# Optimization experiments

Measured on AMD Instinct MI355X. Metric: run time of the kernel, lower is better.

## Reference

```python
import jax, jax.numpy as jnp
import numpy as np

P = 2.0  # exponent from init kwarg p


def _segment_mean(vals, idx, n):
    # scatter-mean with zero for empty segments (matches torch_scatter reduce='mean')
    s = jax.ops.segment_sum(vals, idx, num_segments=n)
    c = jax.ops.segment_sum(jnp.ones((vals.shape[0], 1), vals.dtype), idx, num_segments=n)
    return s / jnp.maximum(c, 1.0)


def setup_inputs() -> dict:
    key = jax.random.key(0)
    ks = jax.random.split(key, 6)
    N, E, nhid, heads = 100000, 3200000, 64, 4
    X = jax.random.normal(ks[0], (N, nhid), dtype=jnp.float32)
    edge_index = jax.random.randint(ks[1], (2, E), 0, N, dtype=jnp.int32)
    s1 = 1.0 / np.sqrt(nhid)
    W_self = jax.random.normal(ks[2], (nhid, nhid), dtype=jnp.float32) * s1
    W_neigh = jax.random.normal(ks[3], (nhid, nhid), dtype=jnp.float32) * s1
    b_conv = jnp.zeros((nhid,), dtype=jnp.float32)
    s2 = 1.0 / np.sqrt(2 * nhid)
    Qw = jax.random.normal(ks[4], (heads, 2 * nhid, nhid // heads), dtype=jnp.float32) * s2
    Qb = jnp.zeros((heads, nhid // heads), dtype=jnp.float32)
    return {"X": X, "edge_index": edge_index, "W_self": W_self,
            "W_neigh": W_neigh, "b_conv": b_conv, "Qw": Qw, "Qb": Qb}


def reference(X, edge_index, W_self, W_neigh, b_conv, Qw, Qb):
    N = X.shape[0]
    src, dst = edge_index[0], edge_index[1]
    # GraphSAGE conv: self-linear + linear over mean of neighbor features, then ReLU
    agg = _segment_mean(X[src], dst, N)                     # [N, nhid]
    X2 = jax.nn.relu(X @ W_self + agg @ W_neigh + b_conv)   # [N, nhid]
    # gather both edge endpoints and concat
    ef = jnp.concatenate([X2[src], X2[dst]], axis=1)        # [E, 2*nhid]
    # per-head small linear, abs^p, heads concatenated -> [E, nhid]
    h = jnp.einsum('ef,hfd->ehd', ef, Qw) + Qb              # [E, heads, nhid/heads]
    h = (jnp.abs(h) ** P).reshape(ef.shape[0], -1)
    # scatter-mean by source node, tanh
    gg = jnp.tanh(_segment_mean(h, src, N))                 # [N, nhid]
    return gg
```

## Files before the change

### kernel.cpp

```cpp
#include <hip/hip_runtime.h>
#include <math.h>

#define NHID 64
#define NPB 512
#define NPB_SHIFT 9
#define MAXB 256
#define CAP 20480
#define CHUNK 8192

__device__ __forceinline__ float bf_lo(unsigned u) { return __uint_as_float(u << 16); }
__device__ __forceinline__ float bf_hi(unsigned u) { return __uint_as_float(u & 0xffff0000u); }
__device__ __forceinline__ unsigned f2bf(float f) {
    unsigned u = __float_as_uint(f);
    return (u + 0x7fffu + ((u >> 16) & 1u)) >> 16;
}

__global__ __launch_bounds__(256) void k_bucketA(const int* __restrict__ src,
                                                 const int* __restrict__ dst,
                                                 unsigned int* __restrict__ buf0,
                                                 unsigned int* __restrict__ buf1,
                                                 int* __restrict__ btail0,
                                                 int* __restrict__ btail1,
                                                 int E, int nB) {
    int side  = blockIdx.x & 1;
    int chunk = blockIdx.x >> 1;
    const int* key = side ? src : dst;
    const int* pay = side ? dst : src;
    unsigned int* buf = side ? buf1 : buf0;
    int* btail = side ? btail1 : btail0;

    __shared__ int h[MAXB], b[MAXB];
    int tid = threadIdx.x;
    for (int i = tid; i < nB; i += 256) h[i] = 0;
    __syncthreads();
    int e0 = chunk * CHUNK;
    for (int i = tid; i < CHUNK / 4; i += 256) {
        int e = e0 + i * 4;
        if (e + 3 < E) {
            int4 k4 = ((const int4*)(key + e0))[i];
            atomicAdd(&h[k4.x >> NPB_SHIFT], 1);
            atomicAdd(&h[k4.y >> NPB_SHIFT], 1);
            atomicAdd(&h[k4.z >> NPB_SHIFT], 1);
            atomicAdd(&h[k4.w >> NPB_SHIFT], 1);
        } else {
            for (int j = 0; j < 4; ++j) {
                int e2 = e + j;
                if (e2 < E) atomicAdd(&h[key[e2] >> NPB_SHIFT], 1);
            }
        }
    }
    __syncthreads();
    for (int i = tid; i < nB; i += 256) {
        int c = h[i];
        b[i] = c ? atomicAdd(&btail[i], c) : 0;
        h[i] = 0;
    }
    __syncthreads();
    for (int i = tid; i < CHUNK / 4; i += 256) {
        int e = e0 + i * 4;
        if (e + 3 < E) {
            int4 k4 = ((const int4*)(key + e0))[i];
            int4 p4 = ((const int4*)(pay + e0))[i];
            int bb, r;
            bb = k4.x >> NPB_SHIFT; r = atomicAdd(&h[bb], 1) + b[bb];
            if (r < CAP) buf[(size_t)bb * CAP + r] = ((unsigned)p4.x << NPB_SHIFT) | (unsigned)(k4.x & (NPB - 1));
            bb = k4.y >> NPB_SHIFT; r = atomicAdd(&h[bb], 1) + b[bb];
            if (r < CAP) buf[(size_t)bb * CAP + r] = ((unsigned)p4.y << NPB_SHIFT) | (unsigned)(k4.y & (NPB - 1));
            bb = k4.z >> NPB_SHIFT; r = atomicAdd(&h[bb], 1) + b[bb];
            if (r < CAP) buf[(size_t)bb * CAP + r] = ((unsigned)p4.z << NPB_SHIFT) | (unsigned)(k4.z & (NPB - 1));
            bb = k4.w >> NPB_SHIFT; r = atomicAdd(&h[bb], 1) + b[bb];
            if (r < CAP) buf[(size_t)bb * CAP + r] = ((unsigned)p4.w << NPB_SHIFT) | (unsigned)(k4.w & (NPB - 1));
        } else {
            for (int j = 0; j < 4; ++j) {
                int e2 = e + j;
                if (e2 < E) {
                    int k = key[e2], p = pay[e2];
                    int bb = k >> NPB_SHIFT;
                    int r = atomicAdd(&h[bb], 1) + b[bb];
                    if (r < CAP) buf[(size_t)bb * CAP + r] = ((unsigned)p << NPB_SHIFT) | (unsigned)(k & (NPB - 1));
                }
            }
        }
    }
}

__global__ __launch_bounds__(256) void k_bscan(const int* __restrict__ btail0,
                                               const int* __restrict__ btail1,
                                               int* __restrict__ boff0, int* __restrict__ boff1,
                                               int* __restrict__ off0, int* __restrict__ off1,
                                               int nB, int N) {
    __shared__ int sd[256];
    int tid = threadIdx.x;
    int v = (tid < nB) ? min(btail0[tid], CAP) : 0;
    sd[tid] = v; __syncthreads();
    for (int o = 1; o < 256; o <<= 1) {
        int t = (tid >= o) ? sd[tid - o] : 0; __syncthreads();
        sd[tid] += t; __syncthreads();
    }
    if (tid < nB) boff0[tid] = sd[tid] - v;
    if (tid == 255) off0[N] = sd[255];
    __syncthreads();
    v = (tid < nB) ? min(btail1[tid], CAP) : 0;
    sd[tid] = v; __syncthreads();
    for (int o = 1; o < 256; o <<= 1) {
        int t = (tid >= o) ? sd[tid - o] : 0; __syncthreads();
        sd[tid] += t; __syncthreads();
    }
    if (tid < nB) boff1[tid] = sd[tid] - v;
    if (tid == 255) off1[N] = sd[255];
}

__global__ __launch_bounds__(512) void k_bucket_csr(const unsigned int* __restrict__ buf0,
                                                    const unsigned int* __restrict__ buf1,
                                                    const int* __restrict__ btail0,
                                                    const int* __restrict__ btail1,
                                                    const int* __restrict__ boff0,
                                                    const int* __restrict__ boff1,
                                                    int* __restrict__ off0, int* __restrict__ off1,
                                                    int* __restrict__ csr0, int* __restrict__ csr1,
                                                    int N) {
    int side = blockIdx.x & 1;
    int b = blockIdx.x >> 1;
    const unsigned int* buf = (side ? buf1 : buf0) + (size_t)b * CAP;
    int cnt_b = min((side ? btail1 : btail0)[b], CAP);
    int boff  = (side ? boff1 : boff0)[b];
    int* off  = side ? off1 : off0;
    int* csr  = side ? csr1 : csr0;
    __shared__ int cnt[NPB];
    __shared__ int scn[NPB];
    __shared__ int cur[NPB];
    int tid = threadIdx.x;
    cnt[tid] = 0;
    __syncthreads();
    for (int i = tid; i < cnt_b; i += 512)
        atomicAdd(&cnt[buf[i] & (NPB - 1)], 1);
    __syncthreads();
    int v = cnt[tid];
    scn[tid] = v; __syncthreads();
    for (int o = 1; o < 512; o <<= 1) {
        int t = (tid >= o) ? scn[tid - o] : 0; __syncthreads();
        scn[tid] += t; __syncthreads();
    }
    int base = boff + scn[tid] - v;
    cur[tid] = base;
    int node = (b << NPB_SHIFT) + tid;
    if (node < N) off[node] = base;
    __syncthreads();
    for (int i = tid; i < cnt_b; i += 512) {
        unsigned int u = buf[i];
        int pos = atomicAdd(&cur[u & (NPB - 1)], 1);
        csr[pos] = (int)(u >> NPB_SHIFT);
    }
}

__global__ __launch_bounds__(256) void k_xcast(const float* __restrict__ X,
                                               unsigned* __restrict__ Xb, int total8) {
    int i = blockIdx.x * 256 + threadIdx.x;
    if (i >= total8) return;
    const float4* Xv = (const float4*)X;
    float4 f0 = Xv[(size_t)i * 2];
    float4 f1 = Xv[(size_t)i * 2 + 1];
    uint4 p;
    p.x = f2bf(f0.x) | (f2bf(f0.y) << 16);
    p.y = f2bf(f0.z) | (f2bf(f0.w) << 16);
    p.z = f2bf(f1.x) | (f2bf(f1.y) << 16);
    p.w = f2bf(f1.z) | (f2bf(f1.w) << 16);
    ((uint4*)Xb)[i] = p;
}

#define AGG_ACC(u) \
    accA.x += bf_lo(u.x); accA.y += bf_hi(u.x); \
    accA.z += bf_lo(u.y); accA.w += bf_hi(u.y); \
    accB.x += bf_lo(u.z); accB.y += bf_hi(u.z); \
    accB.z += bf_lo(u.w); accB.w += bf_hi(u.w);
#define AGG_ACCM(u, f) \
    accA.x += f * bf_lo(u.x); accA.y += f * bf_hi(u.x); \
    accA.z += f * bf_lo(u.y); accA.w += f * bf_hi(u.y); \
    accB.x += f * bf_lo(u.z); accB.y += f * bf_hi(u.z); \
    accB.z += f * bf_lo(u.w); accB.w += f * bf_hi(u.w);

__global__ __launch_bounds__(256) void k_agg(const unsigned* __restrict__ Xb,
                                             const int* __restrict__ off_dst,
                                             const int* __restrict__ csr_dst,
                                             float* __restrict__ agg, int N) {
    int lane = threadIdx.x & 63;
    int node = blockIdx.x * 4 + (threadIdx.x >> 6);
    if (node >= N) return;
    int grp = lane >> 3, col8 = lane & 7;
    const uint4* Xb4 = (const uint4*)Xb;
    int s0 = off_dst[node], s1 = off_dst[node + 1];
    float4 accA = make_float4(0.f, 0.f, 0.f, 0.f);
    float4 accB = make_float4(0.f, 0.f, 0.f, 0.f);
    for (int base = s0; base < s1; base += 64) {
        int cnt = min(64, s1 - base);
        int idx = (base + lane < s1) ? csr_dst[base + lane] : 0;
        int j = 0;
        for (; j + 32 <= cnt; j += 32) {
            int m0 = __shfl(idx, j + grp);
            int m1 = __shfl(idx, j + 8 + grp);
            int m2 = __shfl(idx, j + 16 + grp);
            int m3 = __shfl(idx, j + 24 + grp);
            uint4 u0 = Xb4[(size_t)m0 * 8 + col8];
            uint4 u1 = Xb4[(size_t)m1 * 8 + col8];
            uint4 u2 = Xb4[(size_t)m2 * 8 + col8];
            uint4 u3 = Xb4[(size_t)m3 * 8 + col8];
            AGG_ACC(u0); AGG_ACC(u1); AGG_ACC(u2); AGG_ACC(u3);
        }
        if (j < cnt) {
            int q0 = j + grp, q1 = j + 8 + grp, q2 = j + 16 + grp, q3 = j + 24 + grp;
            int m0 = __shfl(idx, q0);
            int m1 = __shfl(idx, q1);
            int m2 = __shfl(idx, q2);
            int m3 = __shfl(idx, q3);
            float f0 = (q0 < cnt) ? 1.f : 0.f; if (q0 >= cnt) m0 = 0;
            float f1 = (q1 < cnt) ? 1.f : 0.f; if (q1 >= cnt) m1 = 0;
            float f2 = (q2 < cnt) ? 1.f : 0.f; if (q2 >= cnt) m2 = 0;
            float f3 = (q3 < cnt) ? 1.f : 0.f; if (q3 >= cnt) m3 = 0;
            uint4 u0 = Xb4[(size_t)m0 * 8 + col8];
            uint4 u1 = Xb4[(size_t)m1 * 8 + col8];
            uint4 u2 = Xb4[(size_t)m2 * 8 + col8];
            uint4 u3 = Xb4[(size_t)m3 * 8 + col8];
            AGG_ACCM(u0, f0); AGG_ACCM(u1, f1); AGG_ACCM(u2, f2); AGG_ACCM(u3, f3);
        }
    }
    #pragma unroll
    for (int d = 8; d < 64; d <<= 1) {
        accA.x += __shfl_xor(accA.x, d); accA.y += __shfl_xor(accA.y, d);
        accA.z += __shfl_xor(accA.z, d); accA.w += __shfl_xor(accA.w, d);
        accB.x += __shfl_xor(accB.x, d); accB.y += __shfl_xor(accB.y, d);
        accB.z += __shfl_xor(accB.z, d); accB.w += __shfl_xor(accB.w, d);
    }
    if (grp == 0) {
        int deg = s1 - s0;
        float inv = 1.f / (float)max(deg, 1);
        float4 r0 = make_float4(accA.x * inv, accA.y * inv, accA.z * inv, accA.w * inv);
        float4 r1 = make_float4(accB.x * inv, accB.y * inv, accB.z * inv, accB.w * inv);
        ((float4*)agg)[(size_t)node * 16 + col8 * 2]     = r0;
        ((float4*)agg)[(size_t)node * 16 + col8 * 2 + 1] = r1;
    }
}

__global__ __launch_bounds__(256) void k_phaseA(const float* __restrict__ X,
                                                const float* __restrict__ agg,
                                                const float* __restrict__ Ws,
                                                const float* __restrict__ Wn,
                                                const float* __restrict__ bconv,
                                                unsigned* __restrict__ X2b, int N) {
    __shared__ float sWs[4096];
    __shared__ float sWn[4096];
    __shared__ float sb[64];
    int tid = threadIdx.x;
    for (int i = tid; i < 4096; i += 256) {
        sWs[i] = Ws[i];
        sWn[i] = Wn[i];
    }
    if (tid < 64) sb[tid] = bconv[tid];
    __syncthreads();

    int n = blockIdx.x * 64 + (tid >> 2);
    if (n >= N) return;
    int wb = (tid & 3) << 2;
    const float4* ws4 = (const float4*)sWs;
    const float4* wn4 = (const float4*)sWn;
    const float4* bv  = (const float4*)sb;
    const float4* Xv  = (const float4*)(X + (size_t)n * NHID);
    const float4* Gv  = (const float4*)(agg + (size_t)n * NHID);
    float4 a0 = bv[wb], a1 = bv[wb + 1], a2 = bv[wb + 2], a3 = bv[wb + 3];
    #pragma unroll 2
    for (int q = 0; q < 16; ++q) {
        float4 xq = Xv[q];
        float4 gq = Gv[q];
        float xs[4] = {xq.x, xq.y, xq.z, xq.w};
        float gs[4] = {gq.x, gq.y, gq.z, gq.w};
        #pragma unroll
        for (int j = 0; j < 4; ++j) {
            int k16 = (4 * q + j) * 16 + wb;
            float4 w0 = ws4[k16], w1 = ws4[k16 + 1], w2 = ws4[k16 + 2], w3 = ws4[k16 + 3];
            float4 m0 = wn4[k16], m1 = wn4[k16 + 1], m2 = wn4[k16 + 2], m3 = wn4[k16 + 3];
            float xj = xs[j], gj = gs[j];
            a0.x += xj * w0.x + gj * m0.x; a0.y += xj * w0.y + gj * m0.y;
            a0.z += xj * w0.z + gj * m0.z; a0.w += xj * w0.w + gj * m0.w;
            a1.x += xj * w1.x + gj * m1.x; a1.y += xj * w1.y + gj * m1.y;
            a1.z += xj * w1.z + gj * m1.z; a1.w += xj * w1.w + gj * m1.w;
            a2.x += xj * w2.x + gj * m2.x; a2.y += xj * w2.y + gj * m2.y;
            a2.z += xj * w2.z + gj * m2.z; a2.w += xj * w2.w + gj * m2.w;
            a3.x += xj * w3.x + gj * m3.x; a3.y += xj * w3.y + gj * m3.y;
            a3.z += xj * w3.z + gj * m3.z; a3.w += xj * w3.w + gj * m3.w;
        }
    }
    a0.x = fmaxf(a0.x, 0.f); a0.y = fmaxf(a0.y, 0.f); a0.z = fmaxf(a0.z, 0.f); a0.w = fmaxf(a0.w, 0.f);
    a1.x = fmaxf(a1.x, 0.f); a1.y = fmaxf(a1.y, 0.f); a1.z = fmaxf(a1.z, 0.f); a1.w = fmaxf(a1.w, 0.f);
    a2.x = fmaxf(a2.x, 0.f); a2.y = fmaxf(a2.y, 0.f); a2.z = fmaxf(a2.z, 0.f); a2.w = fmaxf(a2.w, 0.f);
    a3.x = fmaxf(a3.x, 0.f); a3.y = fmaxf(a3.y, 0.f); a3.z = fmaxf(a3.z, 0.f); a3.w = fmaxf(a3.w, 0.f);
    uint4 p0, p1;
    p0.x = f2bf(a0.x) | (f2bf(a0.y) << 16);
    p0.y = f2bf(a0.z) | (f2bf(a0.w) << 16);
    p0.z = f2bf(a1.x) | (f2bf(a1.y) << 16);
    p0.w = f2bf(a1.z) | (f2bf(a1.w) << 16);
    p1.x = f2bf(a2.x) | (f2bf(a2.y) << 16);
    p1.y = f2bf(a2.z) | (f2bf(a2.w) << 16);
    p1.z = f2bf(a3.x) | (f2bf(a3.y) << 16);
    p1.w = f2bf(a3.z) | (f2bf(a3.w) << 16);
    uint4* outp = (uint4*)X2b + (size_t)n * 8 + (tid & 3) * 2;
    outp[0] = p0; outp[1] = p1;
}

__global__ __launch_bounds__(256) void k_repackB(const float* __restrict__ Qw,
                                                 float* __restrict__ W2) {
    int i = blockIdx.x * 256 + threadIdx.x;
    if (i >= 8192) return;
    int f = i >> 7, c = i & 127;
    float v;
    if (c < 64) v = Qw[(c >> 4) * 2048 + f * 16 + (c & 15)];
    else { int cc = c - 64; v = Qw[(cc >> 4) * 2048 + (64 + f) * 16 + (cc & 15)]; }
    W2[i] = v;
}

__global__ __launch_bounds__(256) void k_phaseB(const unsigned* __restrict__ X2b,
                                                const float* __restrict__ W2,
                                                const float* __restrict__ Qb,
                                                unsigned* __restrict__ aOut,
                                                unsigned* __restrict__ bOut, int N) {
    __shared__ float sW[10240];
    int tid = threadIdx.x;
    for (int i = tid; i < 8192; i += 256) {
        int f = i >> 7, c = i & 127;
        sW[f * 160 + (c >> 4) * 20 + (c & 15)] = W2[i];
    }
    __syncthreads();

    int n = blockIdx.x * 32 + (tid >> 3);
    if (n >= N) return;
    int part = tid & 7;
    const float4* w4 = (const float4*)sW;
    float4 a0, a1, a2, a3;
    if (part < 4) {
        const float4* qv = (const float4*)Qb;
        int wb = part << 2;
        a0 = qv[wb]; a1 = qv[wb + 1]; a2 = qv[wb + 2]; a3 = qv[wb + 3];
    } else {
        a0 = a1 = a2 = a3 = make_float4(0.f, 0.f, 0.f, 0.f);
    }
    const uint4* Xv = (const uint4*)X2b + (size_t)n * 8;
    int pbase = part * 5;
    #pragma unroll 2
    for (int q8 = 0; q8 < 8; ++q8) {
        uint4 xu = Xv[q8];
        float xs[8] = {bf_lo(xu.x), bf_hi(xu.x), bf_lo(xu.y), bf_hi(xu.y),
                       bf_lo(xu.z), bf_hi(xu.z), bf_lo(xu.w), bf_hi(xu.w)};
        #pragma unroll
        for (int j = 0; j < 8; ++j) {
            int b4 = (8 * q8 + j) * 40 + pbase;
            float4 w0 = w4[b4], w1 = w4[b4 + 1], w2 = w4[b4 + 2], w3 = w4[b4 + 3];
            float xj = xs[j];
            a0.x += xj * w0.x; a0.y += xj * w0.y; a0.z += xj * w0.z; a0.w += xj * w0.w;
            a1.x += xj * w1.x; a1.y += xj * w1.y; a1.z += xj * w1.z; a1.w += xj * w1.w;
            a2.x += xj * w2.x; a2.y += xj * w2.y; a2.z += xj * w2.z; a2.w += xj * w2.w;
            a3.x += xj * w3.x; a3.y += xj * w3.y; a3.z += xj * w3.z; a3.w += xj * w3.w;
        }
    }
    uint4 p0, p1;
    p0.x = f2bf(a0.x) | (f2bf(a0.y) << 16);
    p0.y = f2bf(a0.z) | (f2bf(a0.w) << 16);
    p0.z = f2bf(a1.x) | (f2bf(a1.y) << 16);
    p0.w = f2bf(a1.z) | (f2bf(a1.w) << 16);
    p1.x = f2bf(a2.x) | (f2bf(a2.y) << 16);
    p1.y = f2bf(a2.z) | (f2bf(a2.w) << 16);
    p1.z = f2bf(a3.x) | (f2bf(a3.y) << 16);
    p1.w = f2bf(a3.z) | (f2bf(a3.w) << 16);
    uint4* outp = (part < 4) ? (uint4*)aOut + (size_t)n * 8 + part * 2
                             : (uint4*)bOut + (size_t)n * 8 + (part - 4) * 2;
    outp[0] = p0; outp[1] = p1;
}

#define FIN_ACC(u) { float t; \
    t = avA.x + bf_lo(u.x); accA.x += t * t; \
    t = avA.y + bf_hi(u.x); accA.y += t * t; \
    t = avA.z + bf_lo(u.y); accA.z += t * t; \
    t = avA.w + bf_hi(u.y); accA.w += t * t; \
    t = avB.x + bf_lo(u.z); accB.x += t * t; \
    t = avB.y + bf_hi(u.z); accB.y += t * t; \
    t = avB.z + bf_lo(u.w); accB.z += t * t; \
    t = avB.w + bf_hi(u.w); accB.w += t * t; }
#define FIN_ACCM(u, f) { float t; \
    t = avA.x + bf_lo(u.x); accA.x += f * t * t; \
    t = avA.y + bf_hi(u.x); accA.y += f * t * t; \
    t = avA.z + bf_lo(u.y); accA.z += f * t * t; \
    t = avA.w + bf_hi(u.y); accA.w += f * t * t; \
    t = avB.x + bf_lo(u.z); accB.x += f * t * t; \
    t = avB.y + bf_hi(u.z); accB.y += f * t * t; \
    t = avB.z + bf_lo(u.w); accB.z += f * t * t; \
    t = avB.w + bf_hi(u.w); accB.w += f * t * t; }

__global__ __launch_bounds__(256) void k_final(const unsigned* __restrict__ aFb,
                                               const unsigned* __restrict__ bFb,
                                               const int* __restrict__ off_src,
                                               const int* __restrict__ csr_src,
                                               float* __restrict__ out, int N) {
    int lane = threadIdx.x & 63;
    int node = blockIdx.x * 4 + (threadIdx.x >> 6);
    if (node >= N) return;
    int grp = lane >> 3, col8 = lane & 7;
    const uint4* Bv = (const uint4*)bFb;
    uint4 au = ((const uint4*)aFb)[(size_t)node * 8 + col8];
    float4 avA = make_float4(bf_lo(au.x), bf_hi(au.x), bf_lo(au.y), bf_hi(au.y));
    float4 avB = make_float4(bf_lo(au.z), bf_hi(au.z), bf_lo(au.w), bf_hi(au.w));
    int s0 = off_src[node], s1 = off_src[node + 1];
    float4 accA = make_float4(0.f, 0.f, 0.f, 0.f);
    float4 accB = make_float4(0.f, 0.f, 0.f, 0.f);
    for (int base = s0; base < s1; base += 64) {
        int cnt = min(64, s1 - base);
        int idx = (base + lane < s1) ? csr_src[base + lane] : 0;
        int j = 0;
        for (; j + 32 <= cnt; j += 32) {
            int m0 = __shfl(idx, j + grp);
            int m1 = __shfl(idx, j + 8 + grp);
            int m2 = __shfl(idx, j + 16 + grp);
            int m3 = __shfl(idx, j + 24 + grp);
            uint4 u0 = Bv[(size_t)m0 * 8 + col8];
            uint4 u1 = Bv[(size_t)m1 * 8 + col8];
            uint4 u2 = Bv[(size_t)m2 * 8 + col8];
            uint4 u3 = Bv[(size_t)m3 * 8 + col8];
            FIN_ACC(u0); FIN_ACC(u1); FIN_ACC(u2); FIN_ACC(u3);
        }
        if (j < cnt) {
            int q0 = j + grp, q1 = j + 8 + grp, q2 = j + 16 + grp, q3 = j + 24 + grp;
            int m0 = __shfl(idx, q0);
            int m1 = __shfl(idx, q1);
            int m2 = __shfl(idx, q2);
            int m3 = __shfl(idx, q3);
            float f0 = (q0 < cnt) ? 1.f : 0.f; if (q0 >= cnt) m0 = 0;
            float f1 = (q1 < cnt) ? 1.f : 0.f; if (q1 >= cnt) m1 = 0;
            float f2 = (q2 < cnt) ? 1.f : 0.f; if (q2 >= cnt) m2 = 0;
            float f3 = (q3 < cnt) ? 1.f : 0.f; if (q3 >= cnt) m3 = 0;
            uint4 u0 = Bv[(size_t)m0 * 8 + col8];
            uint4 u1 = Bv[(size_t)m1 * 8 + col8];
            uint4 u2 = Bv[(size_t)m2 * 8 + col8];
            uint4 u3 = Bv[(size_t)m3 * 8 + col8];
            FIN_ACCM(u0, f0); FIN_ACCM(u1, f1); FIN_ACCM(u2, f2); FIN_ACCM(u3, f3);
        }
    }
    #pragma unroll
    for (int d = 8; d < 64; d <<= 1) {
        accA.x += __shfl_xor(accA.x, d); accA.y += __shfl_xor(accA.y, d);
        accA.z += __shfl_xor(accA.z, d); accA.w += __shfl_xor(accA.w, d);
        accB.x += __shfl_xor(accB.x, d); accB.y += __shfl_xor(accB.y, d);
        accB.z += __shfl_xor(accB.z, d); accB.w += __shfl_xor(accB.w, d);
    }
    if (grp == 0) {
        int deg = s1 - s0;
        float inv = 1.f / (float)max(deg, 1);
        float4 r0 = make_float4(tanhf(accA.x * inv), tanhf(accA.y * inv),
                                tanhf(accA.z * inv), tanhf(accA.w * inv));
        float4 r1 = make_float4(tanhf(accB.x * inv), tanhf(accB.y * inv),
                                tanhf(accB.z * inv), tanhf(accB.w * inv));
        ((float4*)out)[(size_t)node * 16 + col8 * 2]     = r0;
        ((float4*)out)[(size_t)node * 16 + col8 * 2 + 1] = r1;
    }
}

extern "C" void kernel_launch(void* const* d_in, const int* in_sizes, int n_in,
                              void* d_out, int out_size, void* d_ws, size_t ws_size,
                              hipStream_t stream) {
    const float* X      = (const float*)d_in[0];
    const int*   ei     = (const int*)d_in[1];
    const float* Wself  = (const float*)d_in[2];
    const float* Wneigh = (const float*)d_in[3];
    const float* bconv  = (const float*)d_in[4];
    const float* Qw     = (const float*)d_in[5];
    const float* Qb     = (const float*)d_in[6];

    int N = in_sizes[0] / NHID;
    int E = in_sizes[1] / 2;
    const int* src = ei;
    const int* dst = ei + E;
    int nB = (N + NPB - 1) >> NPB_SHIFT;
    int nChunks = (E + CHUNK - 1) / CHUNK;

    char* ws = (char*)d_ws;
    size_t bufBytes = (size_t)MAXB * CAP * 4;
    size_t NH4 = (size_t)N * NHID * 4;
    size_t NH2 = (size_t)N * NHID * 2;
    unsigned int* buf0 = (unsigned int*)(ws);
    unsigned int* buf1 = (unsigned int*)(ws + bufBytes);
    float*    aggF = (float*)(ws);
    unsigned* X2b  = (unsigned*)(ws + NH4);
    unsigned* aFb  = (unsigned*)(ws + NH4 + NH2);
    unsigned* bFb  = (unsigned*)(ws + NH4 + 2 * NH2);
    unsigned* Xb   = (unsigned*)(ws + NH4 + 3 * NH2);
    size_t pos = NH4 + 4 * NH2;
    if (pos < 2 * bufBytes) pos = 2 * bufBytes;
    pos = (pos + 255) & ~(size_t)255;
    auto alloc = [&](size_t bytes) -> void* {
        void* p = ws + pos;
        pos = (pos + bytes + 255) & ~(size_t)255;
        return p;
    };
    int* csr0   = (int*)alloc((size_t)E * 4);
    int* csr1   = (int*)alloc((size_t)E * 4);
    int* off0   = (int*)alloc((size_t)(N + 1) * 4);
    int* off1   = (int*)alloc((size_t)(N + 1) * 4);
    int* btail0 = (int*)alloc((size_t)MAXB * 4);
    int* btail1 = (int*)alloc((size_t)MAXB * 4);
    int* boff0  = (int*)alloc((size_t)MAXB * 4);
    int* boff1  = (int*)alloc((size_t)MAXB * 4);
    float* W2   = (float*)alloc((size_t)8192 * 4);
    (void)ws_size; (void)n_in; (void)out_size;

    hipMemsetAsync(btail0, 0, (size_t)2 * MAXB * 4, stream);

    k_bucketA<<<nChunks * 2, 256, 0, stream>>>(src, dst, buf0, buf1, btail0, btail1, E, nB);
    k_bscan<<<1, 256, 0, stream>>>(btail0, btail1, boff0, boff1, off0, off1, nB, N);
    k_repackB<<<32, 256, 0, stream>>>(Qw, W2);
    k_xcast<<<(N * 8 + 255) / 256, 256, 0, stream>>>(X, Xb, N * 8);
    k_bucket_csr<<<nB * 2, 512, 0, stream>>>(buf0, buf1, btail0, btail1,
                                             boff0, boff1, off0, off1, csr0, csr1, N);
    k_agg<<<(N + 3) / 4, 256, 0, stream>>>(Xb, off0, csr0, aggF, N);
    k_phaseA<<<(N + 63) / 64, 256, 0, stream>>>(X, aggF, Wself, Wneigh, bconv, X2b, N);
    k_phaseB<<<(N + 31) / 32, 256, 0, stream>>>(X2b, W2, Qb, aFb, bFb, N);
    k_final<<<(N + 3) / 4, 256, 0, stream>>>(aFb, bFb, off1, csr1, (float*)d_out, N);
}
```

Measured before the change: 320.5 us.

## Merge setup kernels, overlap src-side CSR with aggregation, store agg/X as bf16

Folds the X bf16 cast and Qw repack into the bucketing kernel as extra blocks, and caches keys in shared memory so the second pass does not reload them from global. The src-side CSR build now runs as extra blocks inside the aggregation kernel, so it overlaps with the neighbour mean. The aggregated features are stored in bf16, and phaseA reads bf16 X and agg instead of fp32, which halves those transfers. This reduces launches and memory traffic at the cost of more bf16 rounding in the first layer and a 32KB shared key buffer that may lower occupancy.

After: 328.8 us. +2.6%, slower.

```diff
diff --git a/kernel.cpp b/kernel.cpp
--- a/kernel.cpp
+++ b/kernel.cpp
@@ -15,39 +15,81 @@
     return (u + 0x7fffu + ((u >> 16) & 1u)) >> 16;
 }
 
-__global__ __launch_bounds__(256) void k_bucketA(const int* __restrict__ src,
-                                                 const int* __restrict__ dst,
-                                                 unsigned int* __restrict__ buf0,
-                                                 unsigned int* __restrict__ buf1,
-                                                 int* __restrict__ btail0,
-                                                 int* __restrict__ btail1,
-                                                 int E, int nB) {
-    int side  = blockIdx.x & 1;
-    int chunk = blockIdx.x >> 1;
+__global__ __launch_bounds__(256) void k_build(const int* __restrict__ src,
+                                               const int* __restrict__ dst,
+                                               unsigned int* __restrict__ buf0,
+                                               unsigned int* __restrict__ buf1,
+                                               int* __restrict__ btail0,
+                                               int* __restrict__ btail1,
+                                               const float* __restrict__ X,
+                                               unsigned* __restrict__ Xb,
+                                               const float* __restrict__ Qw,
+                                               float* __restrict__ W2,
+                                               int E, int nB, int nBucketBlocks,
+                                               int nXcastBlocks, int N) {
+    __shared__ int h[MAXB], b[MAXB];
+    __shared__ int sk[CHUNK];
+    int bid = blockIdx.x;
+    int tid = threadIdx.x;
+
+    if (bid >= nBucketBlocks) {
+        int xb = bid - nBucketBlocks;
+        if (xb < nXcastBlocks) {
+            int i = xb * 256 + tid;
+            if (i < N * 8) {
+                const float4* Xv = (const float4*)X;
+                float4 f0 = Xv[(size_t)i * 2];
+                float4 f1 = Xv[(size_t)i * 2 + 1];
+                uint4 p;
+                p.x = f2bf(f0.x) | (f2bf(f0.y) << 16);
+                p.y = f2bf(f0.z) | (f2bf(f0.w) << 16);
+                p.z = f2bf(f1.x) | (f2bf(f1.y) << 16);
+                p.w = f2bf(f1.z) | (f2bf(f1.w) << 16);
+                ((uint4*)Xb)[i] = p;
+            }
+        } else {
+            int i = (xb - nXcastBlocks) * 256 + tid;
+            if (i < 8192) {
+                int f = i >> 7, c = i & 127;
+                float v;
+                if (c < 64) v = Qw[(c >> 4) * 2048 + f * 16 + (c & 15)];
+                else { int cc = c - 64; v = Qw[(cc >> 4) * 2048 + (64 + f) * 16 + (cc & 15)]; }
+                W2[i] = v;
+            }
+        }
+        return;
+    }
+
+    int side  = bid & 1;
+    int chunk = bid >> 1;
     const int* key = side ? src : dst;
     const int* pay = side ? dst : src;
     unsigned int* buf = side ? buf1 : buf0;
     int* btail = side ? btail1 : btail0;
 
-    __shared__ int h[MAXB], b[MAXB];
-    int tid = threadIdx.x;
     for (int i = tid; i < nB; i += 256) h[i] = 0;
     __syncthreads();
     int e0 = chunk * CHUNK;
     for (int i = tid; i < CHUNK / 4; i += 256) {
         int e = e0 + i * 4;
+        int4 k4;
         if (e + 3 < E) {
-            int4 k4 = ((const int4*)(key + e0))[i];
+            k4 = ((const int4*)(key + e0))[i];
             atomicAdd(&h[k4.x >> NPB_SHIFT], 1);
             atomicAdd(&h[k4.y >> NPB_SHIFT], 1);
             atomicAdd(&h[k4.z >> NPB_SHIFT], 1);
             atomicAdd(&h[k4.w >> NPB_SHIFT], 1);
         } else {
-            for (int j = 0; j < 4; ++j) {
-                int e2 = e + j;
-                if (e2 < E) atomicAdd(&h[key[e2] >> NPB_SHIFT], 1);
-            }
-        }
+            k4.x = (e     < E) ? key[e]     : 0;
+            k4.y = (e + 1 < E) ? key[e + 1] : 0;
+            k4.z = (e + 2 < E) ? key[e + 2] : 0;
+            k4.w = (e + 3 < E) ? key[e + 3] : 0;
+            if (e     < E) atomicAdd(&h[k4.x >> NPB_SHIFT], 1);
+            if (e + 1 < E) atomicAdd(&h[k4.y >> NPB_SHIFT], 1);
+            if (e + 2 < E) atomicAdd(&h[k4.z >> NPB_SHIFT], 1);
+            if (e + 3 < E) atomicAdd(&h[k4.w >> NPB_SHIFT], 1);
+        }
+        ((int4*)sk)[i] = k4;
     }
     __syncthreads();
     for (int i = tid; i < nB; i += 256) {
@@ -58,8 +100,8 @@
     __syncthreads();
     for (int i = tid; i < CHUNK / 4; i += 256) {
         int e = e0 + i * 4;
+        int4 k4 = ((const int4*)sk)[i];
         if (e + 3 < E) {
-            int4 k4 = ((const int4*)(key + e0))[i];
             int4 p4 = ((const int4*)(pay + e0))[i];
             int bb, r;
             bb = k4.x >> NPB_SHIFT; r = atomicAdd(&h[bb], 1) + b[bb];
@@ -71,10 +113,11 @@
             bb = k4.w >> NPB_SHIFT; r = atomicAdd(&h[bb], 1) + b[bb];
             if (r < CAP) buf[(size_t)bb * CAP + r] = ((unsigned)p4.w << NPB_SHIFT) | (unsigned)(k4.w & (NPB - 1));
         } else {
+            int ks[4] = {k4.x, k4.y, k4.z, k4.w};
             for (int j = 0; j < 4; ++j) {
                 int e2 = e + j;
                 if (e2 < E) {
-                    int k = key[e2], p = pay[e2];
+                    int k = ks[j], p = pay[e2];
                     int bb = k >> NPB_SHIFT;
                     int r = atomicAdd(&h[bb], 1) + b[bb];
                     if (r < CAP) buf[(size_t)bb * CAP + r] = ((unsigned)p << NPB_SHIFT) | (unsigned)(k & (NPB - 1));
@@ -110,22 +153,9 @@
     if (tid == 255) off1[N] = sd[255];
 }
 
-__global__ __launch_bounds__(512) void k_bucket_csr(const unsigned int* __restrict__ buf0,
-                                                    const unsigned int* __restrict__ buf1,
-                                                    const int* __restrict__ btail0,
-                                                    const int* __restrict__ btail1,
-                                                    const int* __restrict__ boff0,
-                                                    const int* __restrict__ boff1,
-                                                    int* __restrict__ off0, int* __restrict__ off1,
-                                                    int* __restrict__ csr0, int* __restrict__ csr1,
-                                                    int N) {
-    int side = blockIdx.x & 1;
-    int b = blockIdx.x >> 1;
-    const unsigned int* buf = (side ? buf1 : buf0) + (size_t)b * CAP;
-    int cnt_b = min((side ? btail1 : btail0)[b], CAP);
-    int boff  = (side ? boff1 : boff0)[b];
-    int* off  = side ? off1 : off0;
-    int* csr  = side ? csr1 : csr0;
+__device__ void csr_work(const unsigned int* __restrict__ bufb, int cnt_b, int boff,
+                         int* __restrict__ off, int* __restrict__ csr,
+                         int N, int bucket) {
     __shared__ int cnt[NPB];
     __shared__ int scn[NPB];
     __shared__ int cur[NPB];
@@ -133,7 +163,7 @@
     cnt[tid] = 0;
     __syncthreads();
     for (int i = tid; i < cnt_b; i += 512)
-        atomicAdd(&cnt[buf[i] & (NPB - 1)], 1);
+        atomicAdd(&cnt[bufb[i] & (NPB - 1)], 1);
     __syncthreads();
     int v = cnt[tid];
     scn[tid] = v; __syncthreads();
@@ -143,29 +173,23 @@
     }
     int base = boff + scn[tid] - v;
     cur[tid] = base;
-    int node = (b << NPB_SHIFT) + tid;
+    int node = (bucket << NPB_SHIFT) + tid;
     if (node < N) off[node] = base;
     __syncthreads();
     for (int i = tid; i < cnt_b; i += 512) {
-        unsigned int u = buf[i];
+        unsigned int u = bufb[i];
         int pos = atomicAdd(&cur[u & (NPB - 1)], 1);
         csr[pos] = (int)(u >> NPB_SHIFT);
     }
 }
 
-__global__ __launch_bounds__(256) void k_xcast(const float* __restrict__ X,
-                                               unsigned* __restrict__ Xb, int total8) {
-    int i = blockIdx.x * 256 + threadIdx.x;
-    if (i >= total8) return;
-    const float4* Xv = (const float4*)X;
-    float4 f0 = Xv[(size_t)i * 2];
-    float4 f1 = Xv[(size_t)i * 2 + 1];
-    uint4 p;
-    p.x = f2bf(f0.x) | (f2bf(f0.y) << 16);
-    p.y = f2bf(f0.z) | (f2bf(f0.w) << 16);
-    p.z = f2bf(f1.x) | (f2bf(f1.y) << 16);
-    p.w = f2bf(f1.z) | (f2bf(f1.w) << 16);
-    ((uint4*)Xb)[i] = p;
+__global__ __launch_bounds__(512) void k_csr0(const unsigned int* __restrict__ buf0,
+                                              const int* __restrict__ btail0,
+                                              const int* __restrict__ boff0,
+                                              int* __restrict__ off0,
+                                              int* __restrict__ csr0, int N) {
+    int b = blockIdx.x;
+    csr_work(buf0 + (size_t)b * CAP, min(btail0[b], CAP), boff0[b], off0, csr0, N, b);
 }
 
 #define AGG_ACC(u) \
@@ -179,12 +203,25 @@
     accB.x += f * bf_lo(u.z); accB.y += f * bf_hi(u.z); \
     accB.z += f * bf_lo(u.w); accB.w += f * bf_hi(u.w);
 
-__global__ __launch_bounds__(256) void k_agg(const unsigned* __restrict__ Xb,
-                                             const int* __restrict__ off_dst,
-                                             const int* __restrict__ csr_dst,
-                                             float* __restrict__ agg, int N) {
-    int lane = threadIdx.x & 63;
-    int node = blockIdx.x * 4 + (threadIdx.x >> 6);
+__global__ __launch_bounds__(512) void k_aggcsr(const unsigned* __restrict__ Xb,
+                                                const int* __restrict__ off_dst,
+                                                const int* __restrict__ csr_dst,
+                                                unsigned* __restrict__ aggb,
+                                                const unsigned int* __restrict__ buf1,
+                                                const int* __restrict__ btail1,
+                                                const int* __restrict__ boff1,
+                                                int* __restrict__ off1,
+                                                int* __restrict__ csr1,
+                                                int N, int aggBlocks) {
+    int bid = blockIdx.x;
+    if (bid >= aggBlocks) {
+        int b = bid - aggBlocks;
+        csr_work(buf1 + (size_t)b * CAP, min(btail1[b], CAP), boff1[b], off1, csr1, N, b);
+        return;
+    }
+    int tid = threadIdx.x;
+    int lane = tid & 63;
+    int node = bid * 8 + (tid >> 6);
     if (node >= N) return;
     int grp = lane >> 3, col8 = lane & 7;
     const uint4* Xb4 = (const uint4*)Xb;
@@ -233,15 +270,17 @@
     if (grp == 0) {
         int deg = s1 - s0;
         float inv = 1.f / (float)max(deg, 1);
-        float4 r0 = make_float4(accA.x * inv, accA.y * inv, accA.z * inv, accA.w * inv);
-        float4 r1 = make_float4(accB.x * inv, accB.y * inv, accB.z * inv, accB.w * inv);
-        ((float4*)agg)[(size_t)node * 16 + col8 * 2]     = r0;
-        ((float4*)agg)[(size_t)node * 16 + col8 * 2 + 1] = r1;
-    }
-}
-
-__global__ __launch_bounds__(256) void k_phaseA(const float* __restrict__ X,
-                                                const float* __restrict__ agg,
+        uint4 p;
+        p.x = f2bf(accA.x * inv) | (f2bf(accA.y * inv) << 16);
+        p.y = f2bf(accA.z * inv) | (f2bf(accA.w * inv) << 16);
+        p.z = f2bf(accB.x * inv) | (f2bf(accB.y * inv) << 16);
+        p.w = f2bf(accB.z * inv) | (f2bf(accB.w * inv) << 16);
+        ((uint4*)aggb)[(size_t)node * 8 + col8] = p;
+    }
+}
+
+__global__ __launch_bounds__(256) void k_phaseA(const unsigned* __restrict__ Xb,
+                                                const unsigned* __restrict__ aggb,
                                                 const float* __restrict__ Ws,
                                                 const float* __restrict__ Wn,
                                                 const float* __restrict__ bconv,
@@ -263,18 +302,20 @@
     const float4* ws4 = (const float4*)sWs;
     const float4* wn4 = (const float4*)sWn;
     const float4* bv  = (const float4*)sb;
-    const float4* Xv  = (const float4*)(X + (size_t)n * NHID);
-    const float4* Gv  = (const float4*)(agg + (size_t)n * NHID);
+    const uint4* Xv  = (const uint4*)Xb + (size_t)n * 8;
+    const uint4* Gv  = (const uint4*)aggb + (size_t)n * 8;
     float4 a0 = bv[wb], a1 = bv[wb + 1], a2 = bv[wb + 2], a3 = bv[wb + 3];
     #pragma unroll 2
-    for (int q = 0; q < 16; ++q) {
-        float4 xq = Xv[q];
-        float4 gq = Gv[q];
-        float xs[4] = {xq.x, xq.y, xq.z, xq.w};
-        float gs[4] = {gq.x, gq.y, gq.z, gq.w};
+    for (int q8 = 0; q8 < 8; ++q8) {
+        uint4 xu = Xv[q8];
+        uint4 gu = Gv[q8];
+        float xs[8] = {bf_lo(xu.x), bf_hi(xu.x), bf_lo(xu.y), bf_hi(xu.y),
+                       bf_lo(xu.z), bf_hi(xu.z), bf_lo(xu.w), bf_hi(xu.w)};
+        float gs[8] = {bf_lo(gu.x), bf_hi(gu.x), bf_lo(gu.y), bf_hi(gu.y),
+                       bf_lo(gu.z), bf_hi(gu.z), bf_lo(gu.w), bf_hi(gu.w)};
         #pragma unroll
-        for (int j = 0; j < 4; ++j) {
-            int k16 = (4 * q + j) * 16 + wb;
+        for (int j = 0; j < 8; ++j) {
+            int k16 = (8 * q8 + j) * 16 + wb;
             float4 w0 = ws4[k16], w1 = ws4[k16 + 1], w2 = ws4[k16 + 2], w3 = ws4[k16 + 3];
             float4 m0 = wn4[k16], m1 = wn4[k16 + 1], m2 = wn4[k16 + 2], m3 = wn4[k16 + 3];
             float xj = xs[j], gj = gs[j];
@@ -303,17 +344,6 @@
     p1.w = f2bf(a3.z) | (f2bf(a3.w) << 16);
     uint4* outp = (uint4*)X2b + (size_t)n * 8 + (tid & 3) * 2;
     outp[0] = p0; outp[1] = p1;
-}
-
-__global__ __launch_bounds__(256) void k_repackB(const float* __restrict__ Qw,
-                                                 float* __restrict__ W2) {
-    int i = blockIdx.x * 256 + threadIdx.x;
-    if (i >= 8192) return;
-    int f = i >> 7, c = i & 127;
-    float v;
-    if (c < 64) v = Qw[(c >> 4) * 2048 + f * 16 + (c & 15)];
-    else { int cc = c - 64; v = Qw[(cc >> 4) * 2048 + (64 + f) * 16 + (cc & 15)]; }
-    W2[i] = v;
 }
 
 __global__ __launch_bounds__(256) void k_phaseB(const unsigned* __restrict__ X2b,
@@ -479,17 +509,15 @@
 
     char* ws = (char*)d_ws;
     size_t bufBytes = (size_t)MAXB * CAP * 4;
-    size_t NH4 = (size_t)N * NHID * 4;
     size_t NH2 = (size_t)N * NHID * 2;
     unsigned int* buf0 = (unsigned int*)(ws);
     unsigned int* buf1 = (unsigned int*)(ws + bufBytes);
-    float*    aggF = (float*)(ws);
-    unsigned* X2b  = (unsigned*)(ws + NH4);
-    unsigned* aFb  = (unsigned*)(ws + NH4 + NH2);
-    unsigned* bFb  = (unsigned*)(ws + NH4 + 2 * NH2);
-    unsigned* Xb   = (unsigned*)(ws + NH4 + 3 * NH2);
-    size_t pos = NH4 + 4 * NH2;
-    if (pos < 2 * bufBytes) pos = 2 * bufBytes;
+    unsigned* X2b  = (unsigned*)(ws);
+    unsigned* aFb  = (unsigned*)(ws + NH2);
+    unsigned* bFb  = (unsigned*)(ws + 2 * NH2);
+    unsigned* Xb   = (unsigned*)(ws + 2 * bufBytes);
+    unsigned* aggb = (unsigned*)(ws + 2 * bufBytes + NH2);
+    size_t pos = 2 * bufBytes + 2 * NH2;
     pos = (pos + 255) & ~(size_t)255;
     auto alloc = [&](size_t bytes) -> void* {
         void* p = ws + pos;
@@ -509,14 +537,20 @@
 
     hipMemsetAsync(btail0, 0, (size_t)2 * MAXB * 4, stream);
 
-    k_bucketA<<<nChunks * 2, 256, 0, stream>>>(src, dst, buf0, buf1, btail0, btail1, E, nB);
+    int nBucketBlocks = nChunks * 2;
+    int nXcastBlocks  = (N * 8 + 255) / 256;
+    int nBuildBlocks  = nBucketBlocks + nXcastBlocks + 32;
+    int aggBlocks     = (N + 7) / 8;
+
+    k_build<<<nBuildBlocks, 256, 0, stream>>>(src, dst, buf0, buf1, btail0, btail1,
+                                              X, Xb, Qw, W2,
+                                              E, nB, nBucketBlocks, nXcastBlocks, N);
     k_bscan<<<1, 256, 0, stream>>>(btail0, btail1, boff0, boff1, off0, off1, nB, N);
-    k_repackB<<<32, 256, 0, stream>>>(Qw, W2);
-    k_xcast<<<(N * 8 + 255) / 256, 256, 0, stream>>>(X, Xb, N * 8);
-    k_bucket_csr<<<nB * 2, 512, 0, stream>>>(buf0, buf1, btail0, btail1,
-                                             boff0, boff1, off0, off1, csr0, csr1, N);
-    k_agg<<<(N + 3) / 4, 256, 0, stream>>>(Xb, off0, csr0, aggF, N);
-    k_phaseA<<<(N + 63) / 64, 256, 0, stream>>>(X, aggF, Wself, Wneigh, bconv, X2b, N);
+    k_csr0<<<nB, 512, 0, stream>>>(buf0, btail0, boff0, off0, csr0, N);
+    k_aggcsr<<<aggBlocks + nB, 512, 0, stream>>>(Xb, off0, csr0, aggb,
+                                                 buf1, btail1, boff1, off1, csr1,
+                                                 N, aggBlocks);
+    k_phaseA<<<(N + 63) / 64, 256, 0, stream>>>(Xb, aggb, Wself, Wneigh, bconv, X2b, N);
     k_phaseB<<<(N + 31) / 32, 256, 0, stream>>>(X2b, W2, Qb, aFb, bFb, N);
     k_final<<<(N + 3) / 4, 256, 0, stream>>>(aFb, bFb, off1, csr1, (float*)d_out, N);
 }
```
